# Kernel tuning notes

Measured on AMD Instinct MI355X. Metric: run time of the kernel, lower is better.

Reference implementation:

```python
import jax, jax.numpy as jnp
import numpy as np

B, T, H, IN, D = 256, 64, 256, 2, 8

def _gru_cell(x, h, Wih, Whh, bih, bhh):
    gi = x @ Wih.T + bih          # [B,3H]
    gh = h @ Whh.T + bhh
    ir, iz, inn = jnp.split(gi, 3, axis=-1)
    hr, hz, hn = jnp.split(gh, 3, axis=-1)
    r = jax.nn.sigmoid(ir + hr)
    z = jax.nn.sigmoid(iz + hz)
    n = jnp.tanh(inn + r * hn)
    return (1.0 - z) * n + z * h

def _gru2(x, h, p):
    # h: [2,B,H]; p: 8-tuple of layer-0 then layer-1 GRU params
    h0 = _gru_cell(x, h[0], p[0], p[1], p[2], p[3])
    h1 = _gru_cell(h0, h[1], p[4], p[5], p[6], p[7])
    return jnp.stack([h0, h1], axis=0)

def _attend(h_new, buf, i, attn_W, v_W, fc_W, fc_b):
    # h_new: [2,B,H] fresh RNN hidden; buf: [B,T,2,H] history of hiddens
    s = h_new.transpose(1, 0, 2)                            # [B,2,H]
    es = jnp.einsum('blh,gh->blg', s, attn_W[:, :H])        # s half of cat(s,hiddens)
    eh = jnp.einsum('bjlh,gh->bjlg', buf, attn_W[:, H:])    # hiddens half
    energy = jnp.tanh(es[:, None] + eh)                     # [B,T,2,H]
    logits = jnp.einsum('bjlg,og->bjlo', energy, v_W)       # [B,T,2,2]
    mask = (jnp.arange(buf.shape[1]) <= i)[None, :, None, None]
    logits = jnp.where(mask, logits, jnp.float32(-1e30))
    m = logits.max(axis=(1, 2), keepdims=True)              # softmax over all 2*(i+1) history slots
    e = jnp.exp(logits - m)
    a = e / e.sum(axis=(1, 2), keepdims=True)
    c = jnp.einsum('bjlo,bjlh->obh', a, buf)                # [2,B,H] == bmm(a,hiddens).transpose(0,1)
    h_cat = jnp.concatenate([c, h_new], axis=-1)            # [2,B,2H]
    return h_cat @ fc_W.T + fc_b                            # [2,B,H]

def setup_inputs():
    key = jax.random.key(0)
    ks = jax.random.split(key, 32)
    def u(k, shape, fan):
        b = 1.0 / np.sqrt(fan)
        return jax.random.uniform(k, shape, jnp.float32, -b, b)
    inp = {'received': jax.random.normal(ks[0], (B, T, IN), jnp.float32)}
    i = 1
    for g in ('g1', 'g2'):
        inp[g + '_Wih0'] = u(ks[i], (3 * H, IN), H); i += 1
        inp[g + '_Whh0'] = u(ks[i], (3 * H, H), H); i += 1
        inp[g + '_bih0'] = u(ks[i], (3 * H,), H); i += 1
        inp[g + '_bhh0'] = u(ks[i], (3 * H,), H); i += 1
        inp[g + '_Wih1'] = u(ks[i], (3 * H, H), H); i += 1
        inp[g + '_Whh1'] = u(ks[i], (3 * H, H), H); i += 1
        inp[g + '_bih1'] = u(ks[i], (3 * H,), H); i += 1
        inp[g + '_bhh1'] = u(ks[i], (3 * H,), H); i += 1
    inp['fc_W'] = u(ks[i], (H, 2 * H), 2 * H); i += 1
    inp['fc_b'] = u(ks[i], (H,), 2 * H); i += 1
    inp['attn_W'] = u(ks[i], (H, 2 * H), 2 * H); i += 1
    inp['v_W'] = u(ks[i], (2, H), H); i += 1
    inp['out_W'] = u(ks[i], (1, 2 * H), 2 * H); i += 1
    inp['out_b'] = u(ks[i], (1,), 2 * H); i += 1
    return inp

def reference(received, g1_Wih0, g1_Whh0, g1_bih0, g1_bhh0, g1_Wih1, g1_Whh1, g1_bih1, g1_bhh1,
              g2_Wih0, g2_Whh0, g2_bih0, g2_bhh0, g2_Wih1, g2_Whh1, g2_bih1, g2_bhh1,
              fc_W, fc_b, attn_W, v_W, out_W, out_b):
    p1 = (g1_Wih0, g1_Whh0, g1_bih0, g1_bhh0, g1_Wih1, g1_Whh1, g1_bih1, g1_bhh1)
    p2 = (g2_Wih0, g2_Whh0, g2_bih0, g2_bhh0, g2_Wih1, g2_Whh1, g2_bih1, g2_bhh1)
    b, t = received.shape[0], received.shape[1]
    h_init = jnp.zeros((2, b, H), received.dtype)
    buf_init = jnp.zeros((b, t, 2, H), received.dtype)

    def step(carry, inp):
        h1, h2, b1, b2 = carry
        x, i = inp
        h1n = _gru2(x, h1, p1)
        h2n = _gru2(x, h2, p2)
        b1 = b1.at[:, i].set(h1n.transpose(1, 0, 2))
        b2 = b2.at[:, i].set(h2n.transpose(1, 0, 2))
        h1a = _attend(h1n, b1, i, attn_W, v_W, fc_W, fc_b)
        h2a = _attend(h2n, b2, i, attn_W, v_W, fc_W, fc_b)
        return (h1a, h2a, b1, b2), (h1n[1], h2n[1])

    xs = (received.transpose(1, 0, 2), jnp.arange(t))
    _, (o1, o2) = jax.lax.scan(step, (h_init, h_init, buf_init, buf_init), xs)
    out1 = o1.transpose(1, 0, 2)   # [B,T,H] = concat of per-step top-layer GRU outputs
    out2 = o2.transpose(1, 0, 2)
    ar = jnp.arange(t)
    idx = jnp.where(ar >= t - D - 1, t - 1, ar + D)   # delayed stream-2 features
    rnn_out = jnp.concatenate([out1, out2[:, idx]], axis=-1)  # [B,T,2H]
    return jax.nn.sigmoid(rnn_out @ out_W.T + out_b)          # [B,T,1]
```

## Files before the change

### kernel.cpp

```cpp
#include <hip/hip_runtime.h>

#define BATCH 256
#define TT    64
#define HH    256
#define DD    8

#define BW    4
#define NTHR  1024
#define NBLK  (2 * (BATCH / BW))

typedef __attribute__((ext_vector_type(8))) short bfrag;
typedef __attribute__((ext_vector_type(4))) float f4;
typedef __attribute__((ext_vector_type(4))) unsigned int uv4;
typedef __attribute__((ext_vector_type(2))) unsigned int uv2;

#define SWZ(g) ((((g) & 31) << 3) | ((g) >> 5))

__device__ __forceinline__ float rcpf(float x) { return __builtin_amdgcn_rcpf(x); }
__device__ __forceinline__ float sigf(float x) { return rcpf(1.0f + __expf(-x)); }
__device__ __forceinline__ float tanh_fast(float x) {
  const float e = __expf(-2.0f * x);
  return __builtin_fmaf(2.0f, rcpf(1.0f + e), -1.0f);
}
__device__ __forceinline__ unsigned short f2bf(float f) {
  union { float f; unsigned int u; } v; v.f = f;
  return (unsigned short)((v.u + 0x7fffu + ((v.u >> 16) & 1u)) >> 16);
}
__device__ __forceinline__ float bf_lo(unsigned int u) {
  union { unsigned int u; float f; } v; v.u = u << 16; return v.f;
}
__device__ __forceinline__ float bf_hi(unsigned int u) {
  union { unsigned int u; float f; } v; v.u = u & 0xffff0000u; return v.f;
}
__device__ __forceinline__ bfrag zero_frag() {
  bfrag r;
#pragma unroll
  for (int x = 0; x < 8; x++) r[x] = 0;
  return r;
}
__device__ __forceinline__ f4 mfma16(bfrag a, bfrag b, f4 c) {
  return __builtin_amdgcn_mfma_f32_16x16x32_bf16(a, b, c, 0, 0, 0);
}

#define W1_ELEMS  196608
#define STACK_W   (3 * W1_ELEMS)
#define B3_OFF    (2 * STACK_W)
#define B4_OFF    (B3_OFF + 131072)
#define WF_TOTAL  (B4_OFF + 131072)

__global__ __launch_bounds__(256) void prep_weights(
    const float* __restrict__ g1_Whh0, const float* __restrict__ g1_Wih1, const float* __restrict__ g1_Whh1,
    const float* __restrict__ g2_Whh0, const float* __restrict__ g2_Wih1, const float* __restrict__ g2_Whh1,
    const float* __restrict__ attn_W, const float* __restrict__ fc_W,
    unsigned short* __restrict__ wf) {
  const int id = blockIdx.x * 256 + threadIdx.x;
  if (id >= WF_TOTAL) return;
  float src;
  if (id < 2 * STACK_W) {
    const int s = id / STACK_W, r = id % STACK_W;
    const int mm = r / W1_ELEMS, e = r % W1_ELEMS;
    const int j = e & 7, lane = (e >> 3) & 63, c = (e >> 9) & 7, t = e >> 12;
    const int nt = t / 3, g = t % 3;
    const int n = nt * 16 + (lane & 15);
    const int k = c * 32 + ((lane >> 4) << 3) + j;
    const float* W = (mm == 0) ? (s ? g2_Whh0 : g1_Whh0)
                   : (mm == 1) ? (s ? g2_Wih1 : g1_Wih1)
                               : (s ? g2_Whh1 : g1_Whh1);
    src = W[(g * 256 + n) * 256 + k];
  } else if (id < B4_OFF) {
    const int e = id - B3_OFF;
    const int j = e & 7, lane = (e >> 3) & 63, c = (e >> 9) & 7, t = e >> 12;
    const int n = t * 16 + (lane & 15);
    const int k = c * 32 + ((lane >> 4) << 3) + j;
    src = (n < 256) ? attn_W[n * 512 + k] : attn_W[(n - 256) * 512 + 256 + k];
  } else {
    const int e = id - B4_OFF;
    const int j = e & 7, lane = (e >> 3) & 63, c = (e >> 9) & 15, t = e >> 13;
    const int n = t * 16 + (lane & 15);
    const int k = c * 32 + ((lane >> 4) << 3) + j;
    src = fc_W[n * 512 + k];
  }
  wf[id] = f2bf(src);
}

__global__ __launch_bounds__(NTHR) __attribute__((amdgpu_waves_per_eu(4, 4))) void gru_attn(
    const float* __restrict__ received,
    const float* __restrict__ g1_Wih0, const float* __restrict__ g1_bih0, const float* __restrict__ g1_bhh0,
    const float* __restrict__ g1_bih1, const float* __restrict__ g1_bhh1,
    const float* __restrict__ g2_Wih0, const float* __restrict__ g2_bih0, const float* __restrict__ g2_bhh0,
    const float* __restrict__ g2_bih1, const float* __restrict__ g2_bhh1,
    const float* __restrict__ fc_b, const float* __restrict__ v_W, const float* __restrict__ out_W,
    const unsigned short* __restrict__ wf,
    unsigned short* __restrict__ buf_g, unsigned short* __restrict__ ehb_g,
    float* __restrict__ ws_p) {
  const int tid  = threadIdx.x;
  const int lane = tid & 63, wave = tid >> 6;
  const int col  = lane & 15, q = lane >> 4;
  const int s    = blockIdx.x & 1;
  const int b0   = (blockIdx.x >> 1) * BW;

  const float* Wih0 = s ? g2_Wih0 : g1_Wih0;
  const float* bih0 = s ? g2_bih0 : g1_bih0;
  const float* bhh0 = s ? g2_bhh0 : g1_bhh0;
  const float* bih1 = s ? g2_bih1 : g1_bih1;
  const float* bhh1 = s ? g2_bhh1 : g1_bhh1;

  const bfrag* W1  = (const bfrag*)(wf + (size_t)s * STACK_W);
  const bfrag* W2I = W1 + W1_ELEMS / 8;
  const bfrag* W2H = W2I + W1_ELEMS / 8;
  const bfrag* B3  = (const bfrag*)(wf + B3_OFF);
  const bfrag* B4  = (const bfrag*)(wf + B4_OFF);

  unsigned short* buf = buf_g + (size_t)s * BATCH * TT * 2 * HH;
  unsigned short* ehb = ehb_g + (size_t)s * BATCH * TT * 2 * HH;
  float* pp = ws_p + (size_t)s * BATCH * TT;

  const int nm0 = wave * 16 + col;
  const float wxr0 = Wih0[nm0 * 2],         wxr1 = Wih0[nm0 * 2 + 1];
  const float wxz0 = Wih0[(256 + nm0) * 2], wxz1 = Wih0[(256 + nm0) * 2 + 1];
  const float wxn0 = Wih0[(512 + nm0) * 2], wxn1 = Wih0[(512 + nm0) * 2 + 1];
  const float br0  = bih0[nm0] + bhh0[nm0];
  const float bz0  = bih0[256 + nm0] + bhh0[256 + nm0];
  const float bni0 = bih0[512 + nm0], bnh0 = bhh0[512 + nm0];
  const float br1  = bih1[nm0] + bhh1[nm0];
  const float bz1  = bih1[256 + nm0] + bhh1[256 + nm0];
  const float bni1 = bih1[512 + nm0], bnh1 = bhh1[512 + nm0];
  const float fcb  = fc_b[nm0];
  const float owv  = out_W[s * HH + nm0];

  __shared__ float          hf[8 * 260] __attribute__((aligned(16)));
  __shared__ unsigned short hb[8 * 264] __attribute__((aligned(16)));
  __shared__ unsigned short hnb[8 * 264] __attribute__((aligned(16)));
  __shared__ float          es_s[8 * 264] __attribute__((aligned(16)));
  __shared__ unsigned short cacb[8 * 264] __attribute__((aligned(16)));
  __shared__ float          lp[TT * 4 * 2 * 2];
  __shared__ float          vw_s[512];
  __shared__ float          cpart[4 * 2 * 4 * 256] __attribute__((aligned(16)));
  __shared__ float          pw_s[64];
  __shared__ float          sinv_s[8];

  for (int x = tid; x < 8 * 260; x += NTHR) hf[x] = 0.0f;
  for (int x = tid; x < 8 * 264; x += NTHR) hb[x] = 0;
  if (tid < 512) { const int o = tid >> 8, g = tid & 255; vw_s[o * 256 + SWZ(g)] = v_W[tid]; }
  __syncthreads();

#pragma unroll 1
  for (int i = 0; i < TT; ++i) {
    float2 xv[BW];
#pragma unroll
    for (int b = 0; b < BW; b++) xv[b] = ((const float2*)received)[(size_t)(b0 + b) * TT + i];

    {
      bfrag a0[8];
#pragma unroll
      for (int c = 0; c < 8; c++)
        a0[c] = (col < BW) ? *(const bfrag*)&hb[col * 264 + c * 32 + q * 8] : zero_frag();
      const int nt16 = wave;
      bfrag bb[24];
#pragma unroll
      for (int c = 0; c < 8; c++) {
        bb[c]      = W1[((nt16 * 3 + 0) * 8 + c) * 64 + lane];
        bb[8 + c]  = W1[((nt16 * 3 + 1) * 8 + c) * 64 + lane];
        bb[16 + c] = W1[((nt16 * 3 + 2) * 8 + c) * 64 + lane];
      }
      f4 aR = {0, 0, 0, 0}, aZ = {0, 0, 0, 0}, aN = {0, 0, 0, 0};
#pragma unroll
      for (int c = 0; c < 8; c++) {
        aR = mfma16(a0[c], bb[c], aR);
        aZ = mfma16(a0[c], bb[8 + c], aZ);
        aN = mfma16(a0[c], bb[16 + c], aN);
      }
      if (lane < 16) {
#pragma unroll
        for (int reg = 0; reg < 4; reg++) {
          const int b = reg;
          const float rr = sigf(xv[b].x * wxr0 + xv[b].y * wxr1 + br0 + aR[reg]);
          const float zz = sigf(xv[b].x * wxz0 + xv[b].y * wxz1 + bz0 + aZ[reg]);
          const float nn = tanh_fast(xv[b].x * wxn0 + xv[b].y * wxn1 + bni0 +
                                     rr * (aN[reg] + bnh0));
          const float hn0 = (1.0f - zz) * nn + zz * hf[b * 260 + nm0];
          const unsigned short hv = f2bf(hn0);
          hnb[b * 264 + nm0] = hv;
          buf[((size_t)(b0 + b) * (TT * 2) + i * 2 + 0) * HH + nm0] = hv;
        }
      }
    }
    __syncthreads();

    {
      bfrag ai[8], ah[8];
#pragma unroll
      for (int c = 0; c < 8; c++) {
        ai[c] = (col < BW) ? *(const bfrag*)&hnb[col * 264 + c * 32 + q * 8] : zero_frag();
        ah[c] = (col < BW) ? *(const bfrag*)&hb[(4 + col) * 264 + c * 32 + q * 8] : zero_frag();
      }
      float pv[4] = {0.f, 0.f, 0.f, 0.f};
      const int nt16 = wave;
      bfrag bb[24];
#pragma unroll
      for (int c = 0; c < 8; c++) {
        bb[c]      = W2I[((nt16 * 3 + 0) * 8 + c) * 64 + lane];
        bb[8 + c]  = W2I[((nt16 * 3 + 1) * 8 + c) * 64 + lane];
        bb[16 + c] = W2I[((nt16 * 3 + 2) * 8 + c) * 64 + lane];
      }
      f4 iR = {0, 0, 0, 0}, iZ = {0, 0, 0, 0}, iN = {0, 0, 0, 0};
#pragma unroll
      for (int c = 0; c < 8; c++) {
        iR = mfma16(ai[c], bb[c], iR);
        iZ = mfma16(ai[c], bb[8 + c], iZ);
        iN = mfma16(ai[c], bb[16 + c], iN);
      }
#pragma unroll
      for (int c = 0; c < 8; c++) {
        bb[c]      = W2H[((nt16 * 3 + 0) * 8 + c) * 64 + lane];
        bb[8 + c]  = W2H[((nt16 * 3 + 1) * 8 + c) * 64 + lane];
        bb[16 + c] = W2H[((nt16 * 3 + 2) * 8 + c) * 64 + lane];
      }
      f4 hR = {0, 0, 0, 0}, hZ = {0, 0, 0, 0}, hN = {0, 0, 0, 0};
#pragma unroll
      for (int c = 0; c < 8; c++) {
        hR = mfma16(ah[c], bb[c], hR);
        hZ = mfma16(ah[c], bb[8 + c], hZ);
        hN = mfma16(ah[c], bb[16 + c], hN);
      }
      if (lane < 16) {
#pragma unroll
        for (int reg = 0; reg < 4; reg++) {
          const int b = reg;
          const float rr = sigf(iR[reg] + hR[reg] + br1);
          const float zz = sigf(iZ[reg] + hZ[reg] + bz1);
          const float nn = tanh_fast(iN[reg] + bni1 + rr * (hN[reg] + bnh1));
          const float hn1 = (1.0f - zz) * nn + zz * hf[(4 + b) * 260 + nm0];
          const unsigned short hv = f2bf(hn1);
          hnb[(4 + b) * 264 + nm0] = hv;
          buf[((size_t)(b0 + b) * (TT * 2) + i * 2 + 1) * HH + nm0] = hv;
          pv[reg] += hn1 * owv;
        }
      }
#pragma unroll
      for (int reg = 0; reg < 4; reg++) {
#pragma unroll
        for (int d = 1; d < 16; d <<= 1) pv[reg] += __shfl_xor(pv[reg], d, 64);
      }
      if (lane == 0) {
#pragma unroll
        for (int reg = 0; reg < 4; reg++) pw_s[wave * 4 + reg] = pv[reg];
      }
    }
    __syncthreads();

    {
      bfrag a3[8];
#pragma unroll
      for (int c = 0; c < 8; c++)
        a3[c] = (col < 8) ? *(const bfrag*)&hnb[col * 264 + c * 32 + q * 8] : zero_frag();
#pragma unroll
      for (int tt = 0; tt < 2; tt++) {
        const int t = wave * 2 + tt;
        bfrag bb[8];
#pragma unroll
        for (int c = 0; c < 8; c++) bb[c] = B3[(t * 8 + c) * 64 + lane];
        f4 acc = {0, 0, 0, 0};
#pragma unroll
        for (int c = 0; c < 8; c++) acc = mfma16(a3[c], bb[c], acc);
        if (lane < 32) {
          const int n = t * 16 + col;
#pragma unroll
          for (int reg = 0; reg < 4; reg++) {
            const int m = q * 4 + reg;
            const int l = m >> 2, b = m & 3;
            if (t < 16) es_s[(b * 2 + l) * 264 + SWZ(n)] = acc[reg];
            else ehb[((size_t)(b0 + b) * (TT * 2) + i * 2 + l) * HH + (n - 256)] = f2bf(acc[reg]);
          }
        }
      }
      if (tid < 4) {
        float ss = 0.0f;
#pragma unroll
        for (int w = 0; w < 16; w++) ss += pw_s[w * 4 + tid];
        pp[(size_t)(b0 + tid) * TT + i] = ss;
      }
    }
    __syncthreads();

    {
      const int nslot = 64 * (i + 1);
      int slot = tid;
      uv4 cur[4];
      if (slot < nslot) {
        const uv4* ep = (const uv4*)(ehb + ((size_t)(b0 + ((slot >> 3) & 3)) * (TT * 2) +
                                            (slot >> 6) * 2 + ((slot >> 5) & 1)) * HH + (slot & 7) * 32);
#pragma unroll
        for (int u = 0; u < 4; u++) cur[u] = __builtin_nontemporal_load(ep + u);
      }
      for (; slot < nslot; slot += NTHR) {
        const int snext = slot + NTHR;
        uv4 nxt[4];
        if (snext < nslot) {
          const uv4* ep2 = (const uv4*)(ehb + ((size_t)(b0 + ((snext >> 3) & 3)) * (TT * 2) +
                                               (snext >> 6) * 2 + ((snext >> 5) & 1)) * HH + (snext & 7) * 32);
#pragma unroll
          for (int u = 0; u < 4; u++) nxt[u] = __builtin_nontemporal_load(ep2 + u);
        } else {
#pragma unroll
          for (int u = 0; u < 4; u++) nxt[u] = cur[u];
        }
        const int g8 = slot & 7;
        const int b  = (slot >> 3) & 3;
        const int l  = (slot >> 5) & 1;
        const int j  = slot >> 6;
        const int eb = (b * 2 + l) * 264;
        float l0 = 0.0f, l1 = 0.0f;
#pragma unroll
        for (int u = 0; u < 4; u++) {
#pragma unroll
          for (int k = 0; k < 4; k++) {
            const int m = u * 8 + k * 2;
            const float e0 = tanh_fast(es_s[eb + (m * 8 + g8)] + bf_lo(cur[u][k]));
            const float e1 = tanh_fast(es_s[eb + ((m + 1) * 8 + g8)] + bf_hi(cur[u][k]));
            l0 = fmaf(e0, vw_s[m * 8 + g8], fmaf(e1, vw_s[(m + 1) * 8 + g8], l0));
            l1 = fmaf(e0, vw_s[256 + m * 8 + g8], fmaf(e1, vw_s[256 + (m + 1) * 8 + g8], l1));
          }
        }
#pragma unroll
        for (int d = 1; d < 8; d <<= 1) { l0 += __shfl_xor(l0, d, 64); l1 += __shfl_xor(l1, d, 64); }
        if (g8 == 0) {
          lp[((j * 4 + b) * 2 + l) * 2 + 0] = __expf(l0);
          lp[((j * 4 + b) * 2 + l) * 2 + 1] = __expf(l1);
        }
#pragma unroll
        for (int u = 0; u < 4; u++) cur[u] = nxt[u];
      }
    }
    __syncthreads();

    {
      if (wave < 8) {
        const int b = wave >> 1, o = wave & 1;
        const int jl2 = 2 * (i + 1);
        const int jl0 = lane, jl1 = lane + 64;
        float sa = 0.0f;
        if (jl0 < jl2) sa += lp[((jl0 >> 1) * 4 + b) * 4 + (jl0 & 1) * 2 + o];
        if (jl1 < jl2) sa += lp[((jl1 >> 1) * 4 + b) * 4 + (jl1 & 1) * 2 + o];
#pragma unroll
        for (int d = 1; d < 64; d <<= 1) sa += __shfl_xor(sa, d, 64);
        if (lane == 0) sinv_s[b * 2 + o] = rcpf(sa);
      }
      const int h4   = tid & 63;
      const int jpar = (tid >> 6) & 3;
      const int cb   = tid >> 8;
      const uv2* bp = (const uv2*)(buf + ((size_t)(b0 + cb) * (TT * 2)) * HH);
      float c00 = 0.f, c01 = 0.f, c02 = 0.f, c03 = 0.f;
      float c10 = 0.f, c11 = 0.f, c12 = 0.f, c13 = 0.f;
      uv2 aj0 = {0, 0}, aj1 = {0, 0}, bj0 = {0, 0}, bj1 = {0, 0};
      int j = jpar;
      if (j <= i) {
        aj0 = __builtin_nontemporal_load(bp + (j * 2 + 0) * 64 + h4);
        aj1 = __builtin_nontemporal_load(bp + (j * 2 + 1) * 64 + h4);
        bj0 = __builtin_nontemporal_load(bp + ((j + 4) * 2 + 0) * 64 + h4);
        bj1 = __builtin_nontemporal_load(bp + ((j + 4) * 2 + 1) * 64 + h4);
      }
      for (; j <= i; j += 4) {
        uv2 cj0 = {0, 0}, cj1 = {0, 0};
        if (j + 8 <= i) {
          cj0 = __builtin_nontemporal_load(bp + ((j + 8) * 2 + 0) * 64 + h4);
          cj1 = __builtin_nontemporal_load(bp + ((j + 8) * 2 + 1) * 64 + h4);
        }
#pragma unroll
        for (int l = 0; l < 2; l++) {
          const uv2 u = l ? aj1 : aj0;
          const float e0 = lp[((j * 4 + cb) * 2 + l) * 2 + 0];
          const float e1 = lp[((j * 4 + cb) * 2 + l) * 2 + 1];
          const float v0 = bf_lo(u[0]), v1 = bf_hi(u[0]);
          const float v2 = bf_lo(u[1]), v3 = bf_hi(u[1]);
          c00 = fmaf(e0, v0, c00); c01 = fmaf(e0, v1, c01);
          c02 = fmaf(e0, v2, c02); c03 = fmaf(e0, v3, c03);
          c10 = fmaf(e1, v0, c10); c11 = fmaf(e1, v1, c11);
          c12 = fmaf(e1, v2, c12); c13 = fmaf(e1, v3, c13);
        }
        aj0 = bj0; aj1 = bj1; bj0 = cj0; bj1 = cj1;
      }
      ((float4*)&cpart[((jpar * 2 + 0) * 4 + cb) * 256])[h4] = make_float4(c00, c01, c02, c03);
      ((float4*)&cpart[((jpar * 2 + 1) * 4 + cb) * 256])[h4] = make_float4(c10, c11, c12, c13);
    }
    __syncthreads();

    for (int x = tid; x < 2 * BW * HH; x += NTHR) {
      const int g = x & 255, b = (x >> 8) & 3, o = x >> 10;
      const float v = (cpart[((0 * 2 + o) * 4 + b) * 256 + g] +
                       cpart[((1 * 2 + o) * 4 + b) * 256 + g] +
                       cpart[((2 * 2 + o) * 4 + b) * 256 + g] +
                       cpart[((3 * 2 + o) * 4 + b) * 256 + g]) *
                      sinv_s[b * 2 + o];
      cacb[(o * 4 + b) * 264 + g] = f2bf(v);
    }
    __syncthreads();

    {
      bfrag a4[16];
      if (col < 8) {
#pragma unroll
        for (int c = 0; c < 8; c++) {
          a4[c]     = *(const bfrag*)&cacb[col * 264 + c * 32 + q * 8];
          a4[c + 8] = *(const bfrag*)&hnb[col * 264 + c * 32 + q * 8];
        }
      } else {
#pragma unroll
        for (int c = 0; c < 16; c++) a4[c] = zero_frag();
      }
      const int t16 = wave;
      bfrag bb[16];
#pragma unroll
      for (int c = 0; c < 16; c++) bb[c] = B4[(t16 * 16 + c) * 64 + lane];
      f4 acc = {0, 0, 0, 0};
#pragma unroll
      for (int c = 0; c < 16; c++) acc = mfma16(a4[c], bb[c], acc);
      if (lane < 32) {
#pragma unroll
        for (int reg = 0; reg < 4; reg++) {
          const int m = q * 4 + reg;
          const float v = acc[reg] + fcb;
          hf[m * 260 + nm0] = v;
          hb[m * 264 + nm0] = f2bf(v);
        }
      }
    }
    __syncthreads();
  }
}

__global__ __launch_bounds__(256) void final_combine(const float* __restrict__ ws_p,
                                                     const float* __restrict__ out_b,
                                                     float* __restrict__ out) {
  const int gidx = blockIdx.x * blockDim.x + threadIdx.x;
  if (gidx >= BATCH * TT) return;
  const int b = gidx >> 6;
  const int t = gidx & 63;
  const int idx = (t >= TT - DD - 1) ? (TT - 1) : (t + DD);
  const float* p1 = ws_p;
  const float* p2 = ws_p + (size_t)BATCH * TT;
  const float v = p1[(size_t)b * TT + t] + p2[(size_t)b * TT + idx] + out_b[0];
  out[gidx] = 1.0f / (1.0f + __expf(-v));
}

extern "C" void kernel_launch(void* const* d_in, const int* in_sizes, int n_in,
                              void* d_out, int out_size, void* d_ws, size_t ws_size,
                              hipStream_t stream) {
  const float* received = (const float*)d_in[0];
  const float* g1_Wih0 = (const float*)d_in[1];
  const float* g1_Whh0 = (const float*)d_in[2];
  const float* g1_bih0 = (const float*)d_in[3];
  const float* g1_bhh0 = (const float*)d_in[4];
  const float* g1_Wih1 = (const float*)d_in[5];
  const float* g1_Whh1 = (const float*)d_in[6];
  const float* g1_bih1 = (const float*)d_in[7];
  const float* g1_bhh1 = (const float*)d_in[8];
  const float* g2_Wih0 = (const float*)d_in[9];
  const float* g2_Whh0 = (const float*)d_in[10];
  const float* g2_bih0 = (const float*)d_in[11];
  const float* g2_bhh0 = (const float*)d_in[12];
// ... 30 lines not shown
```

Measured before the change: 5.613 ms.

## Stream GRU and attention weights through double-buffered LDS via async global_load_lds

```diff
diff --git a/kernel.cpp b/kernel.cpp
--- a/kernel.cpp
+++ b/kernel.cpp
@@ -9,10 +9,12 @@
 #define NTHR  1024
 #define NBLK  (2 * (BATCH / BW))
 
+#define CH48  24576
+#define CH32  16384
+
 typedef __attribute__((ext_vector_type(8))) short bfrag;
 typedef __attribute__((ext_vector_type(4))) float f4;
 typedef __attribute__((ext_vector_type(4))) unsigned int uv4;
-typedef __attribute__((ext_vector_type(2))) unsigned int uv2;
 
 #define SWZ(g) ((((g) & 31) << 3) | ((g) >> 5))
 
@@ -40,6 +42,39 @@
 }
 __device__ __forceinline__ f4 mfma16(bfrag a, bfrag b, f4 c) {
   return __builtin_amdgcn_mfma_f32_16x16x32_bf16(a, b, c, 0, 0, 0);
+}
+
+__device__ __forceinline__ void wait_vm(int n) {
+  if (n == 0)      asm volatile("s_waitcnt vmcnt(0)" ::: "memory");
+  else if (n == 2) asm volatile("s_waitcnt vmcnt(2)" ::: "memory");
+  else if (n == 3) asm volatile("s_waitcnt vmcnt(3)" ::: "memory");
+  else if (n == 6) asm volatile("s_waitcnt vmcnt(6)" ::: "memory");
+  else             asm volatile("s_waitcnt vmcnt(7)" ::: "memory");
+  __builtin_amdgcn_sched_barrier(0);
+}
+__device__ __forceinline__ void lds_release_bar() {
+  asm volatile("s_waitcnt lgkmcnt(0)" ::: "memory");
+  __builtin_amdgcn_sched_barrier(0);
+  __builtin_amdgcn_s_barrier();
+  __builtin_amdgcn_sched_barrier(0);
+}
+
+__device__ __forceinline__ void gl_lds16(const unsigned short* g, unsigned short* l) {
+  __builtin_amdgcn_global_load_lds(
+      (const __attribute__((address_space(1))) unsigned int*)g,
+      (__attribute__((address_space(3))) unsigned int*)l, 16, 0, 0);
+}
+__device__ __forceinline__ void stage48(const unsigned short* g, unsigned short* l,
+                                        int wave, int lane) {
+#pragma unroll
+  for (int r = 0; r < 3; ++r)
+    gl_lds16(g + wave * 1536 + r * 512 + lane * 8, l + wave * 1536 + r * 512);
+}
+__device__ __forceinline__ void stage32(const unsigned short* g, unsigned short* l,
+                                        int wave, int lane) {
+#pragma unroll
+  for (int r = 0; r < 2; ++r)
+    gl_lds16(g + wave * 1024 + r * 512 + lane * 8, l + wave * 1024 + r * 512);
 }
 
 #define W1_ELEMS  196608
@@ -59,9 +94,11 @@
   if (id < 2 * STACK_W) {
     const int s = id / STACK_W, r = id % STACK_W;
     const int mm = r / W1_ELEMS, e = r % W1_ELEMS;
-    const int j = e & 7, lane = (e >> 3) & 63, c = (e >> 9) & 7, t = e >> 12;
-    const int nt = t / 3, g = t % 3;
-    const int n = nt * 16 + (lane & 15);
+    const int c = e / CH48, e2 = e % CH48;
+    const int wg = e2 >> 9, l8 = e2 & 511;
+    const int w = wg / 3, g = wg % 3;
+    const int lane = l8 >> 3, j = l8 & 7;
+    const int n = w * 16 + (lane & 15);
     const int k = c * 32 + ((lane >> 4) << 3) + j;
     const float* W = (mm == 0) ? (s ? g2_Whh0 : g1_Whh0)
                    : (mm == 1) ? (s ? g2_Wih1 : g1_Wih1)
@@ -69,21 +106,26 @@
     src = W[(g * 256 + n) * 256 + k];
   } else if (id < B4_OFF) {
     const int e = id - B3_OFF;
-    const int j = e & 7, lane = (e >> 3) & 63, c = (e >> 9) & 7, t = e >> 12;
+    const int c = e / CH32, e2 = e % CH32;
+    const int t = e2 >> 9, l8 = e2 & 511;
+    const int lane = l8 >> 3, j = l8 & 7;
     const int n = t * 16 + (lane & 15);
     const int k = c * 32 + ((lane >> 4) << 3) + j;
     src = (n < 256) ? attn_W[n * 512 + k] : attn_W[(n - 256) * 512 + 256 + k];
   } else {
     const int e = id - B4_OFF;
-    const int j = e & 7, lane = (e >> 3) & 63, c = (e >> 9) & 15, t = e >> 13;
-    const int n = t * 16 + (lane & 15);
+    const int cc = e / CH32, e2 = e % CH32;
+    const int w = e2 >> 10, c2 = (e2 >> 9) & 1, l8 = e2 & 511;
+    const int lane = l8 >> 3, j = l8 & 7;
+    const int c = cc * 2 + c2;
+    const int n = w * 16 + (lane & 15);
     const int k = c * 32 + ((lane >> 4) << 3) + j;
     src = fc_W[n * 512 + k];
   }
   wf[id] = f2bf(src);
 }
 
-__global__ __launch_bounds__(NTHR) __attribute__((amdgpu_waves_per_eu(4, 4))) void gru_attn(
+__global__ __launch_bounds__(NTHR) void gru_attn(
     const float* __restrict__ received,
     const float* __restrict__ g1_Wih0, const float* __restrict__ g1_bih0, const float* __restrict__ g1_bhh0,
     const float* __restrict__ g1_bih1, const float* __restrict__ g1_bhh1,
@@ -105,11 +147,9 @@
   const float* bih1 = s ? g2_bih1 : g1_bih1;
   const float* bhh1 = s ? g2_bhh1 : g1_bhh1;
 
-  const bfrag* W1  = (const bfrag*)(wf + (size_t)s * STACK_W);
-  const bfrag* W2I = W1 + W1_ELEMS / 8;
-  const bfrag* W2H = W2I + W1_ELEMS / 8;
-  const bfrag* B3  = (const bfrag*)(wf + B3_OFF);
-  const bfrag* B4  = (const bfrag*)(wf + B4_OFF);
+  const unsigned short* SR = wf + (size_t)s * STACK_W;
+  const unsigned short* B3 = wf + B3_OFF;
+  const unsigned short* B4 = wf + B4_OFF;
 
   unsigned short* buf = buf_g + (size_t)s * BATCH * TT * 2 * HH;
   unsigned short* ehb = ehb_g + (size_t)s * BATCH * TT * 2 * HH;
@@ -135,94 +175,93 @@
   __shared__ unsigned short cacb[8 * 264] __attribute__((aligned(16)));
   __shared__ float          lp[TT * 4 * 2 * 2];
   __shared__ float          vw_s[512];
-  __shared__ float          cpart[4 * 2 * 4 * 256] __attribute__((aligned(16)));
+  __shared__ float          cpart[2 * 2 * 4 * 256] __attribute__((aligned(16)));
   __shared__ float          pw_s[64];
   __shared__ float          sinv_s[8];
+  __shared__ float          xv_s[BW * TT * 2];
+  __shared__ unsigned short wbuf[2][CH48] __attribute__((aligned(16)));
 
   for (int x = tid; x < 8 * 260; x += NTHR) hf[x] = 0.0f;
   for (int x = tid; x < 8 * 264; x += NTHR) hb[x] = 0;
   if (tid < 512) { const int o = tid >> 8, g = tid & 255; vw_s[o * 256 + SWZ(g)] = v_W[tid]; }
+  if (tid < BW * TT * 2) {
+    const int b = tid >> 7, r = tid & 127;
+    xv_s[tid] = received[(size_t)(b0 + b) * TT * 2 + r];
+  }
   __syncthreads();
+
+  stage48(SR + 0 * CH48, wbuf[0], wave, lane);
+  stage48(SR + 1 * CH48, wbuf[1], wave, lane);
 
 #pragma unroll 1
   for (int i = 0; i < TT; ++i) {
-    float2 xv[BW];
-#pragma unroll
-    for (int b = 0; b < BW; b++) xv[b] = ((const float2*)received)[(size_t)(b0 + b) * TT + i];
-
+    f4 aR = {0,0,0,0}, aZ = {0,0,0,0}, aN = {0,0,0,0};
+#pragma unroll
+    for (int c = 0; c < 8; ++c) {
+      wait_vm(3);
+      __builtin_amdgcn_s_barrier();
+      __builtin_amdgcn_sched_barrier(0);
+      const unsigned short* wb = wbuf[c & 1];
+      const bfrag av = (col < BW) ? *(const bfrag*)&hb[col * 264 + c * 32 + q * 8] : zero_frag();
+      const bfrag f0 = *(const bfrag*)&wb[(wave * 3 + 0) * 512 + lane * 8];
+      const bfrag f1 = *(const bfrag*)&wb[(wave * 3 + 1) * 512 + lane * 8];
+      const bfrag f2 = *(const bfrag*)&wb[(wave * 3 + 2) * 512 + lane * 8];
+      aR = mfma16(av, f0, aR); aZ = mfma16(av, f1, aZ); aN = mfma16(av, f2, aN);
+      lds_release_bar();
+      stage48(SR + (c + 2) * CH48, wbuf[c & 1], wave, lane);
+    }
+    if (lane < 16) {
+#pragma unroll
+      for (int reg = 0; reg < 4; reg++) {
+        const int b = reg;
+        const float xr = xv_s[(b * TT + i) * 2 + 0];
+        const float xi = xv_s[(b * TT + i) * 2 + 1];
+        const float rr = sigf(xr * wxr0 + xi * wxr1 + br0 + aR[reg]);
+        const float zz = sigf(xr * wxz0 + xi * wxz1 + bz0 + aZ[reg]);
+        const float nn = tanh_fast(xr * wxn0 + xi * wxn1 + bni0 + rr * (aN[reg] + bnh0));
+        const float hn0 = (1.0f - zz) * nn + zz * hf[b * 260 + nm0];
+        const unsigned short hv = f2bf(hn0);
+        hnb[b * 264 + nm0] = hv;
+        buf[((size_t)(b0 + b) * (TT * 2) + i * 2 + 0) * HH + nm0] = hv;
+      }
+    }
+    lds_release_bar();
+
+    f4 iR = {0,0,0,0}, iZ = {0,0,0,0}, iN = {0,0,0,0};
+#pragma unroll
+    for (int c = 8; c < 16; ++c) {
+      wait_vm(c < 10 ? 7 : 3);
+      __builtin_amdgcn_s_barrier();
+      __builtin_amdgcn_sched_barrier(0);
+      const unsigned short* wb = wbuf[c & 1];
+      const bfrag av = (col < BW) ? *(const bfrag*)&hnb[col * 264 + (c - 8) * 32 + q * 8] : zero_frag();
+      const bfrag f0 = *(const bfrag*)&wb[(wave * 3 + 0) * 512 + lane * 8];
+      const bfrag f1 = *(const bfrag*)&wb[(wave * 3 + 1) * 512 + lane * 8];
+      const bfrag f2 = *(const bfrag*)&wb[(wave * 3 + 2) * 512 + lane * 8];
+      iR = mfma16(av, f0, iR); iZ = mfma16(av, f1, iZ); iN = mfma16(av, f2, iN);
+      lds_release_bar();
+      stage48(SR + (c + 2) * CH48, wbuf[c & 1], wave, lane);
+    }
+
+    f4 hR = {0,0,0,0}, hZ = {0,0,0,0}, hN = {0,0,0,0};
+#pragma unroll
+    for (int c = 16; c < 24; ++c) {
+      wait_vm(c < 23 ? 3 : 0);
+      __builtin_amdgcn_s_barrier();
+      __builtin_amdgcn_sched_barrier(0);
+      const unsigned short* wb = wbuf[c & 1];
+      const bfrag av = (col < BW) ? *(const bfrag*)&hb[(4 + col) * 264 + (c - 16) * 32 + q * 8] : zero_frag();
+      const bfrag f0 = *(const bfrag*)&wb[(wave * 3 + 0) * 512 + lane * 8];
+      const bfrag f1 = *(const bfrag*)&wb[(wave * 3 + 1) * 512 + lane * 8];
+      const bfrag f2 = *(const bfrag*)&wb[(wave * 3 + 2) * 512 + lane * 8];
+      hR = mfma16(av, f0, hR); hZ = mfma16(av, f1, hZ); hN = mfma16(av, f2, hN);
+      lds_release_bar();
+      if (c + 2 < 24) stage48(SR + (c + 2) * CH48, wbuf[c & 1], wave, lane);
+    }
+    stage32(B3 + 0 * CH32, wbuf[0], wave, lane);
+    stage32(B3 + 1 * CH32, wbuf[1], wave, lane);
     {
-      bfrag a0[8];
-#pragma unroll
-      for (int c = 0; c < 8; c++)
-        a0[c] = (col < BW) ? *(const bfrag*)&hb[col * 264 + c * 32 + q * 8] : zero_frag();
-      const int nt16 = wave;
-      bfrag bb[24];
-#pragma unroll
-      for (int c = 0; c < 8; c++) {
-        bb[c]      = W1[((nt16 * 3 + 0) * 8 + c) * 64 + lane];
-        bb[8 + c]  = W1[((nt16 * 3 + 1) * 8 + c) * 64 + lane];
-        bb[16 + c] = W1[((nt16 * 3 + 2) * 8 + c) * 64 + lane];
-      }
-      f4 aR = {0, 0, 0, 0}, aZ = {0, 0, 0, 0}, aN = {0, 0, 0, 0};
-#pragma unroll
-      for (int c = 0; c < 8; c++) {
-        aR = mfma16(a0[c], bb[c], aR);
-        aZ = mfma16(a0[c], bb[8 + c], aZ);
-        aN = mfma16(a0[c], bb[16 + c], aN);
-      }
-      if (lane < 16) {
-#pragma unroll
-        for (int reg = 0; reg < 4; reg++) {
-          const int b = reg;
-          const float rr = sigf(xv[b].x * wxr0 + xv[b].y * wxr1 + br0 + aR[reg]);
-          const float zz = sigf(xv[b].x * wxz0 + xv[b].y * wxz1 + bz0 + aZ[reg]);
-          const float nn = tanh_fast(xv[b].x * wxn0 + xv[b].y * wxn1 + bni0 +
-                                     rr * (aN[reg] + bnh0));
-          const float hn0 = (1.0f - zz) * nn + zz * hf[b * 260 + nm0];
-          const unsigned short hv = f2bf(hn0);
-          hnb[b * 264 + nm0] = hv;
-          buf[((size_t)(b0 + b) * (TT * 2) + i * 2 + 0) * HH + nm0] = hv;
-        }
-      }
-    }
-    __syncthreads();
-
-    {
-      bfrag ai[8], ah[8];
-#pragma unroll
-      for (int c = 0; c < 8; c++) {
-        ai[c] = (col < BW) ? *(const bfrag*)&hnb[col * 264 + c * 32 + q * 8] : zero_frag();
-        ah[c] = (col < BW) ? *(const bfrag*)&hb[(4 + col) * 264 + c * 32 + q * 8] : zero_frag();
-      }
       float pv[4] = {0.f, 0.f, 0.f, 0.f};
-      const int nt16 = wave;
-      bfrag bb[24];
-#pragma unroll
-      for (int c = 0; c < 8; c++) {
-        bb[c]      = W2I[((nt16 * 3 + 0) * 8 + c) * 64 + lane];
-        bb[8 + c]  = W2I[((nt16 * 3 + 1) * 8 + c) * 64 + lane];
-        bb[16 + c] = W2I[((nt16 * 3 + 2) * 8 + c) * 64 + lane];
-      }
-      f4 iR = {0, 0, 0, 0}, iZ = {0, 0, 0, 0}, iN = {0, 0, 0, 0};
-#pragma unroll
-      for (int c = 0; c < 8; c++) {
-        iR = mfma16(ai[c], bb[c], iR);
-        iZ = mfma16(ai[c], bb[8 + c], iZ);
-        iN = mfma16(ai[c], bb[16 + c], iN);
-      }
-#pragma unroll
-      for (int c = 0; c < 8; c++) {
-        bb[c]      = W2H[((nt16 * 3 + 0) * 8 + c) * 64 + lane];
-        bb[8 + c]  = W2H[((nt16 * 3 + 1) * 8 + c) * 64 + lane];
-        bb[16 + c] = W2H[((nt16 * 3 + 2) * 8 + c) * 64 + lane];
-      }
-      f4 hR = {0, 0, 0, 0}, hZ = {0, 0, 0, 0}, hN = {0, 0, 0, 0};
-#pragma unroll
-      for (int c = 0; c < 8; c++) {
-        hR = mfma16(ah[c], bb[c], hR);
-        hZ = mfma16(ah[c], bb[8 + c], hZ);
-        hN = mfma16(ah[c], bb[16 + c], hN);
-      }
       if (lane < 16) {
 #pragma unroll
         for (int reg = 0; reg < 4; reg++) {
@@ -247,22 +286,28 @@
         for (int reg = 0; reg < 4; reg++) pw_s[wave * 4 + reg] = pv[reg];
       }
     }
-    __syncthreads();
+    lds_release_bar();
 
     {
-      bfrag a3[8];
-#pragma unroll
-      for (int c = 0; c < 8; c++)
-        a3[c] = (col < 8) ? *(const bfrag*)&hnb[col * 264 + c * 32 + q * 8] : zero_frag();
+      f4 ac0 = {0,0,0,0}, ac1 = {0,0,0,0};
+#pragma unroll
+      for (int c = 0; c < 8; ++c) {
+        wait_vm(c < 2 ? 6 : (c < 7 ? 2 : 0));
+        __builtin_amdgcn_s_barrier();
+        __builtin_amdgcn_sched_barrier(0);
+        const unsigned short* wb = wbuf[c & 1];
+        const bfrag av = (col < 8) ? *(const bfrag*)&hnb[col * 264 + c * 32 + q * 8] : zero_frag();
+        const bfrag f0 = *(const bfrag*)&wb[(2 * wave + 0) * 512 + lane * 8];
+        const bfrag f1 = *(const bfrag*)&wb[(2 * wave + 1) * 512 + lane * 8];
+        ac0 = mfma16(av, f0, ac0);
+        ac1 = mfma16(av, f1, ac1);
+        lds_release_bar();
+        if (c + 2 < 8) stage32(B3 + (c + 2) * CH32, wbuf[c & 1], wave, lane);
+      }
 #pragma unroll
       for (int tt = 0; tt < 2; tt++) {
+        const f4 acc = tt ? ac1 : ac0;
         const int t = wave * 2 + tt;
-        bfrag bb[8];
-#pragma unroll
-        for (int c = 0; c < 8; c++) bb[c] = B3[(t * 8 + c) * 64 + lane];
-        f4 acc = {0, 0, 0, 0};
-#pragma unroll
-        for (int c = 0; c < 8; c++) acc = mfma16(a3[c], bb[c], acc);
         if (lane < 32) {
           const int n = t * 16 + col;
 #pragma unroll
@@ -346,75 +391,78 @@
         for (int d = 1; d < 64; d <<= 1) sa += __shfl_xor(sa, d, 64);
         if (lane == 0) sinv_s[b * 2 + o] = rcpf(sa);
       }
-      const int h4   = tid & 63;
-      const int jpar = (tid >> 6) & 3;
+      const int h2   = tid & 127;
+      const int jpar = (tid >> 7) & 1;
       const int cb   = tid >> 8;
-      const uv2* bp = (const uv2*)(buf + ((size_t)(b0 + cb) * (TT * 2)) * HH);
-      float c00 = 0.f, c01 = 0.f, c02 = 0.f, c03 = 0.f;
-      float c10 = 0.f, c11 = 0.f, c12 = 0.f, c13 = 0.f;
-      uv2 aj0 = {0, 0}, aj1 = {0, 0}, bj0 = {0, 0}, bj1 = {0, 0};
+      const unsigned int* bp = (const unsigned int*)(buf + ((size_t)(b0 + cb) * (TT * 2)) * HH);
+      float c00 = 0.f, c01 = 0.f, c10 = 0.f, c11 = 0.f;
+      unsigned int aj0 = 0, aj1 = 0, bj0 = 0, bj1 = 0;
       int j = jpar;
       if (j <= i) {
-        aj0 = __builtin_nontemporal_load(bp + (j * 2 + 0) * 64 + h4);
-        aj1 = __builtin_nontemporal_load(bp + (j * 2 + 1) * 64 + h4);
-        bj0 = __builtin_nontemporal_load(bp + ((j + 4) * 2 + 0) * 64 + h4);
-        bj1 = __builtin_nontemporal_load(bp + ((j + 4) * 2 + 1) * 64 + h4);
-      }
-      for (; j <= i; j += 4) {
-        uv2 cj0 = {0, 0}, cj1 = {0, 0};
-        if (j + 8 <= i) {
-          cj0 = __builtin_nontemporal_load(bp + ((j + 8) * 2 + 0) * 64 + h4);
-          cj1 = __builtin_nontemporal_load(bp + ((j + 8) * 2 + 1) * 64 + h4);
+        aj0 = __builtin_nontemporal_load(bp + (j * 2 + 0) * 128 + h2);
+        aj1 = __builtin_nontemporal_load(bp + (j * 2 + 1) * 128 + h2);
+        bj0 = __builtin_nontemporal_load(bp + ((j + 2) * 2 + 0) * 128 + h2);
+        bj1 = __builtin_nontemporal_load(bp + ((j + 2) * 2 + 1) * 128 + h2);
+      }
+      for (; j <= i; j += 2) {
+        unsigned int cj0 = 0, cj1 = 0;
+        if (j + 4 <= i) {
+          cj0 = __builtin_nontemporal_load(bp + ((j + 4) * 2 + 0) * 128 + h2);
+          cj1 = __builtin_nontemporal_load(bp + ((j + 4) * 2 + 1) * 128 + h2);
         }
 #pragma unroll
         for (int l = 0; l < 2; l++) {
-          const uv2 u = l ? aj1 : aj0;
+          const unsigned int u = l ? aj1 : aj0;
           const float e0 = lp[((j * 4 + cb) * 2 + l) * 2 + 0];
           const float e1 = lp[((j * 4 + cb) * 2 + l) * 2 + 1];
-          const float v0 = bf_lo(u[0]), v1 = bf_hi(u[0]);
-          const float v2 = bf_lo(u[1]), v3 = bf_hi(u[1]);
+          const float v0 = bf_lo(u), v1 = bf_hi(u);
           c00 = fmaf(e0, v0, c00); c01 = fmaf(e0, v1, c01);
-          c02 = fmaf(e0, v2, c02); c03 = fmaf(e0, v3, c03);
           c10 = fmaf(e1, v0, c10); c11 = fmaf(e1, v1, c11);
-          c12 = fmaf(e1, v2, c12); c13 = fmaf(e1, v3, c13);
         }
         aj0 = bj0; aj1 = bj1; bj0 = cj0; bj1 = cj1;
       }
-      ((float4*)&cpart[((jpar * 2 + 0) * 4 + cb) * 256])[h4] = make_float4(c00, c01, c02, c03);
-      ((float4*)&cpart[((jpar * 2 + 1) * 4 + cb) * 256])[h4] = make_float4(c10, c11, c12, c13);
+      ((float2*)&cpart[((jpar * 2 + 0) * 4 + cb) * 256])[h2] = make_float2(c00, c01);
+      ((float2*)&cpart[((jpar * 2 + 1) * 4 + cb) * 256])[h2] = make_float2(c10, c11);
     }
     __syncthreads();
 
+    stage32(B4 + 0 * CH32, wbuf[0], wave, lane);
+    stage32(B4 + 1 * CH32, wbuf[1], wave, lane);
     for (int x = tid; x < 2 * BW * HH; x += NTHR) {
       const int g = x & 255, b = (x >> 8) & 3, o = x >> 10;
       const float v = (cpart[((0 * 2 + o) * 4 + b) * 256 + g] +
-                       cpart[((1 * 2 + o) * 4 + b) * 256 + g] +
-                       cpart[((2 * 2 + o) * 4 + b) * 256 + g] +
-                       cpart[((3 * 2 + o) * 4 + b) * 256 + g]) *
+                       cpart[((1 * 2 + o) * 4 + b) * 256 + g]) *
                       sinv_s[b * 2 + o];
       cacb[(o * 4 + b) * 264 + g] = f2bf(v);
     }
     __syncthreads();
 
     {
-      bfrag a4[16];
-      if (col < 8) {
-#pragma unroll
-        for (int c = 0; c < 8; c++) {
-          a4[c]     = *(const bfrag*)&cacb[col * 264 + c * 32 + q * 8];
-          a4[c + 8] = *(const bfrag*)&hnb[col * 264 + c * 32 + q * 8];
-        }
-      } else {
-#pragma unroll
-        for (int c = 0; c < 16; c++) a4[c] = zero_frag();
-      }
-      const int t16 = wave;
-      bfrag bb[16];
-#pragma unroll
-      for (int c = 0; c < 16; c++) bb[c] = B4[(t16 * 16 + c) * 64 + lane];
       f4 acc = {0, 0, 0, 0};
 #pragma unroll
-      for (int c = 0; c < 16; c++) acc = mfma16(a4[c], bb[c], acc);
+      for (int cc = 0; cc < 8; ++cc) {
+        wait_vm(cc < 7 ? 2 : 0);
+        __builtin_amdgcn_s_barrier();
+        __builtin_amdgcn_sched_barrier(0);
+        const unsigned short* wb = wbuf[cc & 1];
+        bfrag a0v, a1v;
+        if (col < 8) {
+          a0v = (cc < 4) ? *(const bfrag*)&cacb[col * 264 + cc * 64 + q * 8]
+                         : *(const bfrag*)&hnb[col * 264 + (cc - 4) * 64 + q * 8];
+          a1v = (cc < 4) ? *(const bfrag*)&cacb[col * 264 + cc * 64 + 32 + q * 8]
+                         : *(const bfrag*)&hnb[col * 264 + (cc - 4) * 64 + 32 + q * 8];
+        } else { a0v = zero_frag(); a1v = zero_frag(); }
+        const bfrag g0 = *(const bfrag*)&wb[(wave * 2 + 0) * 512 + lane * 8];
+        const bfrag g1 = *(const bfrag*)&wb[(wave * 2 + 1) * 512 + lane * 8];
+        acc = mfma16(a0v, g0, acc);
+        acc = mfma16(a1v, g1, acc);
+        lds_release_bar();
+        if (cc + 2 < 8) stage32(B4 + (cc + 2) * CH32, wbuf[cc & 1], wave, lane);
+      }
+      if (i + 1 < TT) {
+        stage48(SR + 0 * CH48, wbuf[0], wave, lane);
+        stage48(SR + 1 * CH48, wbuf[1], wave, lane);
+      }
       if (lane < 32) {
 #pragma unroll
         for (int reg = 0; reg < 4; reg++) {
@@ -425,7 +473,7 @@
         }
       }
     }
-    __syncthreads();
+    lds_release_bar();
   }
 }
 
```

Result: slower. 6.193 ms (+10.3%).

## Halve batch per block and keep attention key history in LDS

Applied to the files above, without the earlier changes.

```diff
diff --git a/kernel.cpp b/kernel.cpp
--- a/kernel.cpp
+++ b/kernel.cpp
@@ -5,14 +5,13 @@
 #define HH    256
 #define DD    8
 
-#define BW    4
+#define BW    2
 #define NTHR  1024
 #define NBLK  (2 * (BATCH / BW))
 
 typedef __attribute__((ext_vector_type(8))) short bfrag;
 typedef __attribute__((ext_vector_type(4))) float f4;
 typedef __attribute__((ext_vector_type(4))) unsigned int uv4;
-typedef __attribute__((ext_vector_type(2))) unsigned int uv2;
 
 #define SWZ(g) ((((g) & 31) << 3) | ((g) >> 5))
 
@@ -83,7 +82,7 @@
   wf[id] = f2bf(src);
 }
 
-__global__ __launch_bounds__(NTHR) __attribute__((amdgpu_waves_per_eu(4, 4))) void gru_attn(
+__global__ __launch_bounds__(NTHR) void gru_attn(
     const float* __restrict__ received,
     const float* __restrict__ g1_Wih0, const float* __restrict__ g1_bih0, const float* __restrict__ g1_bhh0,
     const float* __restrict__ g1_bih1, const float* __restrict__ g1_bhh1,
@@ -112,7 +111,6 @@
   const bfrag* B4  = (const bfrag*)(wf + B4_OFF);
 
   unsigned short* buf = buf_g + (size_t)s * BATCH * TT * 2 * HH;
-  unsigned short* ehb = ehb_g + (size_t)s * BATCH * TT * 2 * HH;
   float* pp = ws_p + (size_t)s * BATCH * TT;
 
   const int nm0 = wave * 16 + col;
@@ -128,19 +126,20 @@
   const float fcb  = fc_b[nm0];
   const float owv  = out_W[s * HH + nm0];
 
-  __shared__ float          hf[8 * 260] __attribute__((aligned(16)));
-  __shared__ unsigned short hb[8 * 264] __attribute__((aligned(16)));
-  __shared__ unsigned short hnb[8 * 264] __attribute__((aligned(16)));
-  __shared__ float          es_s[8 * 264] __attribute__((aligned(16)));
-  __shared__ unsigned short cacb[8 * 264] __attribute__((aligned(16)));
-  __shared__ float          lp[TT * 4 * 2 * 2];
+  float hfr[4] = {0.0f, 0.0f, 0.0f, 0.0f};
+
+  __shared__ unsigned short hb[4 * 264] __attribute__((aligned(16)));
+  __shared__ unsigned short hnb[4 * 264] __attribute__((aligned(16)));
+  __shared__ float          es_s[4 * 264] __attribute__((aligned(16)));
+  __shared__ unsigned short cacb[4 * 264] __attribute__((aligned(16)));
+  __shared__ float          lp[TT * 2 * 2 * 2];
   __shared__ float          vw_s[512];
-  __shared__ float          cpart[4 * 2 * 4 * 256] __attribute__((aligned(16)));
-  __shared__ float          pw_s[64];
-  __shared__ float          sinv_s[8];
-
-  for (int x = tid; x < 8 * 260; x += NTHR) hf[x] = 0.0f;
-  for (int x = tid; x < 8 * 264; x += NTHR) hb[x] = 0;
+  __shared__ float          cpart[4 * 2 * 2 * 256] __attribute__((aligned(16)));
+  __shared__ float          pw_s[32];
+  __shared__ float          sinv_s[4];
+  __shared__ unsigned short eh_lds[TT * 2 * 2 * 256] __attribute__((aligned(16)));
+
+  for (int x = tid; x < 4 * 264; x += NTHR) hb[x] = 0;
   if (tid < 512) { const int o = tid >> 8, g = tid & 255; vw_s[o * 256 + SWZ(g)] = v_W[tid]; }
   __syncthreads();
 
@@ -172,13 +171,13 @@
       }
       if (lane < 16) {
 #pragma unroll
-        for (int reg = 0; reg < 4; reg++) {
+        for (int reg = 0; reg < BW; reg++) {
           const int b = reg;
           const float rr = sigf(xv[b].x * wxr0 + xv[b].y * wxr1 + br0 + aR[reg]);
           const float zz = sigf(xv[b].x * wxz0 + xv[b].y * wxz1 + bz0 + aZ[reg]);
           const float nn = tanh_fast(xv[b].x * wxn0 + xv[b].y * wxn1 + bni0 +
                                      rr * (aN[reg] + bnh0));
-          const float hn0 = (1.0f - zz) * nn + zz * hf[b * 260 + nm0];
+          const float hn0 = (1.0f - zz) * nn + zz * hfr[b];
           const unsigned short hv = f2bf(hn0);
           hnb[b * 264 + nm0] = hv;
           buf[((size_t)(b0 + b) * (TT * 2) + i * 2 + 0) * HH + nm0] = hv;
@@ -192,9 +191,9 @@
 #pragma unroll
       for (int c = 0; c < 8; c++) {
         ai[c] = (col < BW) ? *(const bfrag*)&hnb[col * 264 + c * 32 + q * 8] : zero_frag();
-        ah[c] = (col < BW) ? *(const bfrag*)&hb[(4 + col) * 264 + c * 32 + q * 8] : zero_frag();
-      }
-      float pv[4] = {0.f, 0.f, 0.f, 0.f};
+        ah[c] = (col < BW) ? *(const bfrag*)&hb[(BW + col) * 264 + c * 32 + q * 8] : zero_frag();
+      }
+      float pv[BW] = {0.f, 0.f};
       const int nt16 = wave;
       bfrag bb[24];
 #pragma unroll
@@ -225,26 +224,26 @@
       }
       if (lane < 16) {
 #pragma unroll
-        for (int reg = 0; reg < 4; reg++) {
+        for (int reg = 0; reg < BW; reg++) {
           const int b = reg;
           const float rr = sigf(iR[reg] + hR[reg] + br1);
           const float zz = sigf(iZ[reg] + hZ[reg] + bz1);
           const float nn = tanh_fast(iN[reg] + bni1 + rr * (hN[reg] + bnh1));
-          const float hn1 = (1.0f - zz) * nn + zz * hf[(4 + b) * 260 + nm0];
+          const float hn1 = (1.0f - zz) * nn + zz * hfr[BW + b];
           const unsigned short hv = f2bf(hn1);
-          hnb[(4 + b) * 264 + nm0] = hv;
+          hnb[(BW + b) * 264 + nm0] = hv;
           buf[((size_t)(b0 + b) * (TT * 2) + i * 2 + 1) * HH + nm0] = hv;
           pv[reg] += hn1 * owv;
         }
       }
 #pragma unroll
-      for (int reg = 0; reg < 4; reg++) {
+      for (int reg = 0; reg < BW; reg++) {
 #pragma unroll
         for (int d = 1; d < 16; d <<= 1) pv[reg] += __shfl_xor(pv[reg], d, 64);
       }
       if (lane == 0) {
 #pragma unroll
-        for (int reg = 0; reg < 4; reg++) pw_s[wave * 4 + reg] = pv[reg];
+        for (int reg = 0; reg < BW; reg++) pw_s[wave * BW + reg] = pv[reg];
       }
     }
     __syncthreads();
@@ -253,7 +252,7 @@
       bfrag a3[8];
 #pragma unroll
       for (int c = 0; c < 8; c++)
-        a3[c] = (col < 8) ? *(const bfrag*)&hnb[col * 264 + c * 32 + q * 8] : zero_frag();
+        a3[c] = (col < 2 * BW) ? *(const bfrag*)&hnb[col * 264 + c * 32 + q * 8] : zero_frag();
 #pragma unroll
       for (int tt = 0; tt < 2; tt++) {
         const int t = wave * 2 + tt;
@@ -263,52 +262,36 @@
         f4 acc = {0, 0, 0, 0};
 #pragma unroll
         for (int c = 0; c < 8; c++) acc = mfma16(a3[c], bb[c], acc);
-        if (lane < 32) {
+        if (lane < 16) {
           const int n = t * 16 + col;
 #pragma unroll
           for (int reg = 0; reg < 4; reg++) {
-            const int m = q * 4 + reg;
-            const int l = m >> 2, b = m & 3;
+            const int l = reg >> 1, b = reg & 1;
             if (t < 16) es_s[(b * 2 + l) * 264 + SWZ(n)] = acc[reg];
-            else ehb[((size_t)(b0 + b) * (TT * 2) + i * 2 + l) * HH + (n - 256)] = f2bf(acc[reg]);
+            else eh_lds[(((i * 2 + l) * 2 + b) * 256) + (n - 256)] = f2bf(acc[reg]);
           }
         }
       }
-      if (tid < 4) {
+      if (tid < BW) {
         float ss = 0.0f;
 #pragma unroll
-        for (int w = 0; w < 16; w++) ss += pw_s[w * 4 + tid];
+        for (int w = 0; w < 16; w++) ss += pw_s[w * BW + tid];
         pp[(size_t)(b0 + tid) * TT + i] = ss;
       }
     }
     __syncthreads();
 
     {
-      const int nslot = 64 * (i + 1);
-      int slot = tid;
-      uv4 cur[4];
-      if (slot < nslot) {
-        const uv4* ep = (const uv4*)(ehb + ((size_t)(b0 + ((slot >> 3) & 3)) * (TT * 2) +
-                                            (slot >> 6) * 2 + ((slot >> 5) & 1)) * HH + (slot & 7) * 32);
-#pragma unroll
-        for (int u = 0; u < 4; u++) cur[u] = __builtin_nontemporal_load(ep + u);
-      }
-      for (; slot < nslot; slot += NTHR) {
-        const int snext = slot + NTHR;
-        uv4 nxt[4];
-        if (snext < nslot) {
-          const uv4* ep2 = (const uv4*)(ehb + ((size_t)(b0 + ((snext >> 3) & 3)) * (TT * 2) +
-                                               (snext >> 6) * 2 + ((snext >> 5) & 1)) * HH + (snext & 7) * 32);
-#pragma unroll
-          for (int u = 0; u < 4; u++) nxt[u] = __builtin_nontemporal_load(ep2 + u);
-        } else {
-#pragma unroll
-          for (int u = 0; u < 4; u++) nxt[u] = cur[u];
-        }
+      const int nslot = 32 * (i + 1);
+      for (int slot = tid; slot < nslot; slot += NTHR) {
         const int g8 = slot & 7;
-        const int b  = (slot >> 3) & 3;
-        const int l  = (slot >> 5) & 1;
-        const int j  = slot >> 6;
+        const int b  = (slot >> 3) & 1;
+        const int l  = (slot >> 4) & 1;
+        const int j  = slot >> 5;
+        const unsigned short* ep = &eh_lds[(((j * 2 + l) * 2 + b) * 256) + g8 * 32];
+        uv4 cur[4];
+#pragma unroll
+        for (int u = 0; u < 4; u++) cur[u] = *(const uv4*)(ep + u * 8);
         const int eb = (b * 2 + l) * 264;
         float l0 = 0.0f, l1 = 0.0f;
 #pragma unroll
@@ -325,80 +308,74 @@
 #pragma unroll
         for (int d = 1; d < 8; d <<= 1) { l0 += __shfl_xor(l0, d, 64); l1 += __shfl_xor(l1, d, 64); }
         if (g8 == 0) {
-          lp[((j * 4 + b) * 2 + l) * 2 + 0] = __expf(l0);
-          lp[((j * 4 + b) * 2 + l) * 2 + 1] = __expf(l1);
-        }
-#pragma unroll
-        for (int u = 0; u < 4; u++) cur[u] = nxt[u];
-      }
-    }
-    __syncthreads();
-
-    {
-      if (wave < 8) {
+          lp[((j * 2 + b) * 2 + l) * 2 + 0] = __expf(l0);
+          lp[((j * 2 + b) * 2 + l) * 2 + 1] = __expf(l1);
+        }
+      }
+    }
+    __syncthreads();
+
+    {
+      if (wave < 4) {
         const int b = wave >> 1, o = wave & 1;
         const int jl2 = 2 * (i + 1);
         const int jl0 = lane, jl1 = lane + 64;
         float sa = 0.0f;
-        if (jl0 < jl2) sa += lp[((jl0 >> 1) * 4 + b) * 4 + (jl0 & 1) * 2 + o];
-        if (jl1 < jl2) sa += lp[((jl1 >> 1) * 4 + b) * 4 + (jl1 & 1) * 2 + o];
+        if (jl0 < jl2) sa += lp[(((jl0 >> 1) * 2 + b) * 2 + (jl0 & 1)) * 2 + o];
+        if (jl1 < jl2) sa += lp[(((jl1 >> 1) * 2 + b) * 2 + (jl1 & 1)) * 2 + o];
 #pragma unroll
         for (int d = 1; d < 64; d <<= 1) sa += __shfl_xor(sa, d, 64);
         if (lane == 0) sinv_s[b * 2 + o] = rcpf(sa);
       }
-      const int h4   = tid & 63;
-      const int jpar = (tid >> 6) & 3;
-      const int cb   = tid >> 8;
-      const uv2* bp = (const uv2*)(buf + ((size_t)(b0 + cb) * (TT * 2)) * HH);
-      float c00 = 0.f, c01 = 0.f, c02 = 0.f, c03 = 0.f;
-      float c10 = 0.f, c11 = 0.f, c12 = 0.f, c13 = 0.f;
-      uv2 aj0 = {0, 0}, aj1 = {0, 0}, bj0 = {0, 0}, bj1 = {0, 0};
+      const int h2   = tid & 127;
+      const int jpar = (tid >> 7) & 3;
+      const int cb   = tid >> 9;
+      const unsigned int* bp = (const unsigned int*)(buf + ((size_t)(b0 + cb) * (TT * 2)) * HH);
+      float c00 = 0.f, c01 = 0.f, c10 = 0.f, c11 = 0.f;
+      unsigned int a0v = 0, a1v = 0, b0v = 0, b1v = 0;
       int j = jpar;
       if (j <= i) {
-        aj0 = __builtin_nontemporal_load(bp + (j * 2 + 0) * 64 + h4);
-        aj1 = __builtin_nontemporal_load(bp + (j * 2 + 1) * 64 + h4);
-        bj0 = __builtin_nontemporal_load(bp + ((j + 4) * 2 + 0) * 64 + h4);
-        bj1 = __builtin_nontemporal_load(bp + ((j + 4) * 2 + 1) * 64 + h4);
+        a0v = __builtin_nontemporal_load(bp + (j * 2 + 0) * 128 + h2);
+        a1v = __builtin_nontemporal_load(bp + (j * 2 + 1) * 128 + h2);
+        b0v = __builtin_nontemporal_load(bp + ((j + 4) * 2 + 0) * 128 + h2);
+        b1v = __builtin_nontemporal_load(bp + ((j + 4) * 2 + 1) * 128 + h2);
       }
       for (; j <= i; j += 4) {
-        uv2 cj0 = {0, 0}, cj1 = {0, 0};
+        unsigned int c0v = 0, c1v = 0;
         if (j + 8 <= i) {
-          cj0 = __builtin_nontemporal_load(bp + ((j + 8) * 2 + 0) * 64 + h4);
-          cj1 = __builtin_nontemporal_load(bp + ((j + 8) * 2 + 1) * 64 + h4);
+          c0v = __builtin_nontemporal_load(bp + ((j + 8) * 2 + 0) * 128 + h2);
+          c1v = __builtin_nontemporal_load(bp + ((j + 8) * 2 + 1) * 128 + h2);
         }
 #pragma unroll
         for (int l = 0; l < 2; l++) {
-          const uv2 u = l ? aj1 : aj0;
-          const float e0 = lp[((j * 4 + cb) * 2 + l) * 2 + 0];
-          const float e1 = lp[((j * 4 + cb) * 2 + l) * 2 + 1];
-          const float v0 = bf_lo(u[0]), v1 = bf_hi(u[0]);
-          const float v2 = bf_lo(u[1]), v3 = bf_hi(u[1]);
+          const unsigned int u = l ? a1v : a0v;
+          const float e0 = lp[((j * 2 + cb) * 2 + l) * 2 + 0];
+          const float e1 = lp[((j * 2 + cb) * 2 + l) * 2 + 1];
+          const float v0 = bf_lo(u), v1 = bf_hi(u);
           c00 = fmaf(e0, v0, c00); c01 = fmaf(e0, v1, c01);
-          c02 = fmaf(e0, v2, c02); c03 = fmaf(e0, v3, c03);
           c10 = fmaf(e1, v0, c10); c11 = fmaf(e1, v1, c11);
-          c12 = fmaf(e1, v2, c12); c13 = fmaf(e1, v3, c13);
-        }
-        aj0 = bj0; aj1 = bj1; bj0 = cj0; bj1 = cj1;
-      }
-      ((float4*)&cpart[((jpar * 2 + 0) * 4 + cb) * 256])[h4] = make_float4(c00, c01, c02, c03);
-      ((float4*)&cpart[((jpar * 2 + 1) * 4 + cb) * 256])[h4] = make_float4(c10, c11, c12, c13);
+        }
+        a0v = b0v; a1v = b1v; b0v = c0v; b1v = c1v;
+      }
+      ((float2*)&cpart[((jpar * 2 + 0) * 2 + cb) * 256])[h2] = make_float2(c00, c01);
+      ((float2*)&cpart[((jpar * 2 + 1) * 2 + cb) * 256])[h2] = make_float2(c10, c11);
     }
     __syncthreads();
 
     for (int x = tid; x < 2 * BW * HH; x += NTHR) {
-      const int g = x & 255, b = (x >> 8) & 3, o = x >> 10;
-      const float v = (cpart[((0 * 2 + o) * 4 + b) * 256 + g] +
-                       cpart[((1 * 2 + o) * 4 + b) * 256 + g] +
-                       cpart[((2 * 2 + o) * 4 + b) * 256 + g] +
-                       cpart[((3 * 2 + o) * 4 + b) * 256 + g]) *
+      const int g = x & 255, b = (x >> 8) & 1, o = x >> 9;
+      const float v = (cpart[((0 * 2 + o) * 2 + b) * 256 + g] +
+                       cpart[((1 * 2 + o) * 2 + b) * 256 + g] +
+                       cpart[((2 * 2 + o) * 2 + b) * 256 + g] +
+                       cpart[((3 * 2 + o) * 2 + b) * 256 + g]) *
                       sinv_s[b * 2 + o];
-      cacb[(o * 4 + b) * 264 + g] = f2bf(v);
+      cacb[(o * 2 + b) * 264 + g] = f2bf(v);
     }
     __syncthreads();
 
     {
       bfrag a4[16];
-      if (col < 8) {
+      if (col < 2 * BW) {
 #pragma unroll
         for (int c = 0; c < 8; c++) {
           a4[c]     = *(const bfrag*)&cacb[col * 264 + c * 32 + q * 8];
@@ -415,13 +392,12 @@
       f4 acc = {0, 0, 0, 0};
 #pragma unroll
       for (int c = 0; c < 16; c++) acc = mfma16(a4[c], bb[c], acc);
-      if (lane < 32) {
+      if (lane < 16) {
 #pragma unroll
         for (int reg = 0; reg < 4; reg++) {
-          const int m = q * 4 + reg;
           const float v = acc[reg] + fcb;
-          hf[m * 260 + nm0] = v;
-          hb[m * 264 + nm0] = f2bf(v);
+          hfr[reg] = v;
+          hb[reg * 264 + nm0] = f2bf(v);
         }
       }
     }
```

After: 7.461 ms. 1.33x slower.
